# Kernel tuning notes

Measured on AMD Instinct MI355X. Metric: run time of the kernel, lower is better.

The kernel has to match this reference:

```python
import jax, jax.numpy as jnp
import numpy as np

N = 64       # number of sites / qubits
CHI = 32     # bond dimension chi_max
D = 2        # physical dim (== label dim l)
BATCH = 262144
STD = 0.001  # init noise, matches MPS.initialize_params


def setup_inputs() -> dict:
    key = jax.random.key(0)
    kx, k0, kc, kn = jax.random.split(key, 4)
    # X: [N, batch, d] -- each X[i] contracts with site i's physical leg
    X = jax.random.normal(kx, (N, BATCH, D), dtype=jnp.float32)
    # core0: (d, chi), one-hot column 0 plus noise
    core0 = jnp.zeros((D, CHI), jnp.float32).at[:, 0].set(1.0)
    core0 = core0 + STD * jax.random.normal(k0, (D, CHI), dtype=jnp.float32)
    # middle cores: (N-1, chi, d, chi), identity stacked over d plus noise
    eye = jnp.eye(CHI, dtype=jnp.float32)                      # (chi, chi)
    mid = jnp.broadcast_to(eye[:, None, :], (CHI, D, CHI))     # (chi, d, chi)
    cores = jnp.broadcast_to(mid, (N - 1, CHI, D, CHI))
    cores = cores + STD * jax.random.normal(kc, (N - 1, CHI, D, CHI), dtype=jnp.float32)
    # coreN: (chi, d), one-hot row 0 plus noise
    coreN = jnp.zeros((CHI, D), jnp.float32).at[0].set(1.0)
    coreN = coreN + STD * jax.random.normal(kn, (CHI, D), dtype=jnp.float32)
    return {"X": X, "core0": core0, "cores": cores, "coreN": coreN}


def reference(X, core0, cores, coreN):
    # Sequential MPS chain contraction:
    #   v <- X[0] @ core0                       (batch, chi)
    #   v <- einsum('ab,bqc,aq->ac', v, core_i, X[i])   for i = 1..N-1
    #   out = |v @ coreN|                       (batch, l)
    v0 = jnp.einsum('aq,qc->ac', X[0], core0)  # (B, chi)

    def step(v, inp):
        x, core = inp  # x: (B, d), core: (chi, d, chi)
        # contract bond then physical leg, keeping only (B, chi) resident
        v_new = jnp.einsum('ab,bqc,aq->ac', v, core, x)
        return v_new, None

    v, _ = jax.lax.scan(step, v0, (X[1:], cores))
    out = jnp.einsum('ac,cq->aq', v, coreN)    # (B, l)
    return jnp.abs(out)
```

## Files before the change

kernel.cpp:

```cpp
#include <hip/hip_runtime.h>
#include <hip/hip_bf16.h>

#define BATCH 262144
#define NSITES 64
#define NJ 4
#define BLOCK_BATCH 256

typedef __attribute__((ext_vector_type(8))) short short8;
typedef __attribute__((ext_vector_type(4))) float f32x4;

__device__ __forceinline__ int qmap(int k) {
  return (((k >> 2) & 1) << 4) | (((k >> 3) & 3) << 2) | (k & 3);
}

__global__ void pack_E(const float* __restrict__ cores, unsigned short* __restrict__ Ep) {
  int idx = blockIdx.x * 256 + threadIdx.x;
  if (idx >= (NSITES - 1) * 2048) return;
  int t = idx & 7;
  int l = (idx >> 3) & 63;
  int f = (idx >> 9) & 3;
  int p = idx >> 11;
  int g = l >> 4, col = l & 15;
  int m = f >> 1, h = f & 1;
  int k = 8 * g + t, c = h * 16 + col;
  int b = qmap(k);
  float val = cores[((p * 32 + b) * 2 + m) * 32 + c] - ((b == c) ? 1.0f : 0.0f);
  __hip_bfloat16 hv = __float2bfloat16(val);
  Ep[idx] = *(unsigned short*)&hv;
}

#define BODYJ(jj, xx0, xx1)                                                     \
  {                                                                             \
    union { short8 s8; __hip_bfloat162 h2[4]; } vb;                             \
    vb.h2[0] = __float22bfloat162_rn(make_float2(v[jj][0], v[jj][1]));          \
    vb.h2[1] = __float22bfloat162_rn(make_float2(v[jj][2], v[jj][3]));          \
    vb.h2[2] = __float22bfloat162_rn(make_float2(v[jj][4], v[jj][5]));          \
    vb.h2[3] = __float22bfloat162_rn(make_float2(v[jj][6], v[jj][7]));          \
    const f32x4 z = {0.f, 0.f, 0.f, 0.f};                                       \
    __builtin_amdgcn_s_setprio(1);                                              \
    f32x4 r0lo = __builtin_amdgcn_mfma_f32_16x16x32_bf16(A0, vb.s8, z, 0, 0, 0); \
    f32x4 r0hi = __builtin_amdgcn_mfma_f32_16x16x32_bf16(A1, vb.s8, z, 0, 0, 0); \
    f32x4 r1lo = __builtin_amdgcn_mfma_f32_16x16x32_bf16(A2, vb.s8, z, 0, 0, 0); \
    f32x4 r1hi = __builtin_amdgcn_mfma_f32_16x16x32_bf16(A3, vb.s8, z, 0, 0, 0); \
    __builtin_amdgcn_s_setprio(0);                                              \
    const float ss = (xx0) + (xx1);                                             \
    _Pragma("unroll") for (int t = 0; t < 4; ++t) {                             \
      v[jj][t] = ss * v[jj][t] + (xx0)*r0lo[t] + (xx1)*r1lo[t];                 \
      v[jj][4 + t] = ss * v[jj][4 + t] + (xx0)*r0hi[t] + (xx1)*r1hi[t];         \
    }                                                                           \
  }

__global__ __launch_bounds__(256, 4) void mps_chain_kernel(
    const float* __restrict__ X, const float* __restrict__ core0,
    const float* __restrict__ coreN, const unsigned short* __restrict__ Ep,
    float* __restrict__ out) {
  const int tid = threadIdx.x;
  const int lane = tid & 63;
  const int wave = tid >> 6;
  const int col = lane & 15;
  const int g = lane >> 4;
  const int abase = blockIdx.x * BLOCK_BATCH + wave * (16 * NJ);

  float c0[2][8];
#pragma unroll
  for (int m = 0; m < 2; ++m)
#pragma unroll
    for (int t = 0; t < 8; ++t) c0[m][t] = core0[m * 32 + qmap(8 * g + t)];

  float v[NJ][8];
#pragma unroll
  for (int jj = 0; jj < NJ; ++jj) {
    const float2 xj = *(const float2*)(X + 2 * (size_t)(abase + jj * 16 + col));
#pragma unroll
    for (int t = 0; t < 8; ++t) v[jj][t] = xj.x * c0[0][t] + xj.y * c0[1][t];
  }

  const char* ep_base = (const char*)Ep + (size_t)lane * 16;
  const float* xs = X + 2 * ((size_t)BATCH + abase + col);

#pragma unroll 1
  for (int s = 1; s < NSITES; ++s) {
    const short8* ep = (const short8*)ep_base;
    const short8 A0 = ep[0], A1 = ep[64], A2 = ep[128], A3 = ep[192];

    float2 xj[NJ];
#pragma unroll
    for (int jj = 0; jj < NJ; ++jj)
      xj[jj] = *(const float2*)(xs + 2 * (jj * 16));

    BODYJ(0, xj[0].x, xj[0].y);
    BODYJ(1, xj[1].x, xj[1].y);
    BODYJ(2, xj[2].x, xj[2].y);
    BODYJ(3, xj[3].x, xj[3].y);

    ep_base += 4096;
    xs += 2 * (size_t)BATCH;
  }

  float cN[8][2];
#pragma unroll
  for (int t = 0; t < 8; ++t) {
    cN[t][0] = coreN[qmap(8 * g + t) * 2 + 0];
    cN[t][1] = coreN[qmap(8 * g + t) * 2 + 1];
  }
#pragma unroll
  for (int jj = 0; jj < NJ; ++jj) {
    float p0 = 0.f, p1 = 0.f;
#pragma unroll
    for (int t = 0; t < 8; ++t) {
      p0 += v[jj][t] * cN[t][0];
      p1 += v[jj][t] * cN[t][1];
    }
    p0 += __shfl_xor(p0, 16);
    p0 += __shfl_xor(p0, 32);
    p1 += __shfl_xor(p1, 16);
    p1 += __shfl_xor(p1, 32);
    if (g == 0) {
      const int a = abase + jj * 16 + col;
      out[2 * a] = fabsf(p0);
      out[2 * a + 1] = fabsf(p1);
    }
  }
}

extern "C" void kernel_launch(void* const* d_in, const int* in_sizes, int n_in,
                              void* d_out, int out_size, void* d_ws, size_t ws_size,
                              hipStream_t stream) {
  const float* X = (const float*)d_in[0];
  const float* core0 = (const float*)d_in[1];
  const float* cores = (const float*)d_in[2];
  const float* coreN = (const float*)d_in[3];
  float* out = (float*)d_out;
  unsigned short* Ep = (unsigned short*)d_ws;

  hipLaunchKernelGGL(pack_E, dim3(((NSITES - 1) * 2048 + 255) / 256), dim3(256), 0, stream,
                     cores, Ep);
  hipLaunchKernelGGL(mps_chain_kernel, dim3(BATCH / BLOCK_BATCH), dim3(256), 0, stream, X,
                     core0, coreN, Ep, out);
}
```

Measured before the change: 99.75 us.

## Double-buffer per-site cores and X into LDS via async global_load_lds

Each wave now prefetches the next site's packed bf16 core fragments and its X values into a per-wave double-buffered LDS region using global_load_lds. A manual vmcnt wait means each iteration only waits for the previous stage's loads. The goal is to hide the global-load latency that the unroll-1 site loop previously exposed on every step. In exchange it adds about 36KB of LDS per block, which may limit occupancy, and it depends on hand-placed waitcnt ordering.

```diff
diff --git a/kernel.cpp b/kernel.cpp
--- a/kernel.cpp
+++ b/kernel.cpp
@@ -29,6 +29,17 @@
   Ep[idx] = *(unsigned short*)&hv;
 }
 
+__device__ __forceinline__ void gll16(const void* g, void* l) {
+  __builtin_amdgcn_global_load_lds(
+      (const __attribute__((address_space(1))) unsigned*)g,
+      (__attribute__((address_space(3))) unsigned*)l, 16, 0, 0);
+}
+__device__ __forceinline__ void gll4(const void* g, void* l) {
+  __builtin_amdgcn_global_load_lds(
+      (const __attribute__((address_space(1))) unsigned*)g,
+      (__attribute__((address_space(3))) unsigned*)l, 4, 0, 0);
+}
+
 #define BODYJ(jj, xx0, xx1)                                                     \
   {                                                                             \
     union { short8 s8; __hip_bfloat162 h2[4]; } vb;                             \
@@ -54,12 +65,27 @@
     const float* __restrict__ X, const float* __restrict__ core0,
     const float* __restrict__ coreN, const unsigned short* __restrict__ Ep,
     float* __restrict__ out) {
+  __shared__ __align__(16) char Lds[4][2][4608];
   const int tid = threadIdx.x;
   const int lane = tid & 63;
   const int wave = tid >> 6;
   const int col = lane & 15;
   const int g = lane >> 4;
   const int abase = blockIdx.x * BLOCK_BATCH + wave * (16 * NJ);
+  const char* Epc = (const char*)Ep;
+  const char* Xc = (const char*)X;
+
+#define STAGE(t_, b_)                                                           \
+  {                                                                             \
+    const char* es_ = Epc + (size_t)((t_)-1) * 4096 + (size_t)lane * 16;        \
+    gll16(es_, &Lds[wave][b_][0]);                                              \
+    gll16(es_ + 1024, &Lds[wave][b_][1024]);                                    \
+    gll16(es_ + 2048, &Lds[wave][b_][2048]);                                    \
+    gll16(es_ + 3072, &Lds[wave][b_][3072]);                                    \
+    const char* xs_ = Xc + ((size_t)(t_)*BATCH + abase + lane) * 8;             \
+    gll4(xs_, &Lds[wave][b_][4096]);                                            \
+    gll4(xs_ + 4, &Lds[wave][b_][4352]);                                        \
+  }
 
   float c0[2][8];
 #pragma unroll
@@ -75,26 +101,32 @@
     for (int t = 0; t < 8; ++t) v[jj][t] = xj.x * c0[0][t] + xj.y * c0[1][t];
   }
 
-  const char* ep_base = (const char*)Ep + (size_t)lane * 16;
-  const float* xs = X + 2 * ((size_t)BATCH + abase + col);
+  STAGE(1, 1);
 
 #pragma unroll 1
   for (int s = 1; s < NSITES; ++s) {
-    const short8* ep = (const short8*)ep_base;
+    const int rb = s & 1;
+    if (s + 1 < NSITES) {
+      STAGE(s + 1, rb ^ 1);
+      asm volatile("s_waitcnt vmcnt(6)" ::: "memory");
+    } else {
+      asm volatile("s_waitcnt vmcnt(0)" ::: "memory");
+    }
+
+    const short8* ep = (const short8*)&Lds[wave][rb][lane * 16];
     const short8 A0 = ep[0], A1 = ep[64], A2 = ep[128], A3 = ep[192];
+    const float* xp = (const float*)&Lds[wave][rb][4096];
+    float xv0[NJ], xv1[NJ];
+#pragma unroll
+    for (int jj = 0; jj < NJ; ++jj) {
+      xv0[jj] = xp[jj * 16 + col];
+      xv1[jj] = xp[64 + jj * 16 + col];
+    }
 
-    float2 xj[NJ];
-#pragma unroll
-    for (int jj = 0; jj < NJ; ++jj)
-      xj[jj] = *(const float2*)(xs + 2 * (jj * 16));
-
-    BODYJ(0, xj[0].x, xj[0].y);
-    BODYJ(1, xj[1].x, xj[1].y);
-    BODYJ(2, xj[2].x, xj[2].y);
-    BODYJ(3, xj[3].x, xj[3].y);
-
-    ep_base += 4096;
-    xs += 2 * (size_t)BATCH;
+    BODYJ(0, xv0[0], xv1[0]);
+    BODYJ(1, xv0[1], xv1[1]);
+    BODYJ(2, xv0[2], xv1[2]);
+    BODYJ(3, xv0[3], xv1[3]);
   }
 
   float cN[8][2];
@@ -121,6 +153,7 @@
       out[2 * a + 1] = fabsf(p1);
     }
   }
+#undef STAGE
 }
 
 extern "C" void kernel_launch(void* const* d_in, const int* in_sizes, int n_in,
```

Measured after the change: 104.4 us. 1.05x slower.

## Prefetch next site's X and vectorize state update with packed float2 math

Applied to the files above, without the earlier changes.

Loads the X inputs for site s+1 at the top of each iteration, so global-load latency overlaps the current site's MFMA and update work rather than stalling before it. The per-lane state is also restructured into float2 vectors so the scale-and-accumulate update can map to packed FP32 instructions (v_pk_fma/v_pk_mul). This costs extra registers for the prefetched values, which may press on the 4-waves occupancy bound. It also issues one redundant clamped load on the last iteration.

```diff
diff --git a/kernel.cpp b/kernel.cpp
--- a/kernel.cpp
+++ b/kernel.cpp
@@ -8,6 +8,10 @@
 
 typedef __attribute__((ext_vector_type(8))) short short8;
 typedef __attribute__((ext_vector_type(4))) float f32x4;
+typedef __attribute__((ext_vector_type(2))) float f32x2;
+
+#define LOH2(r) (__builtin_shufflevector((r), (r), 0, 1))
+#define HIH2(r) (__builtin_shufflevector((r), (r), 2, 3))
 
 __device__ __forceinline__ int qmap(int k) {
   return (((k >> 2) & 1) << 4) | (((k >> 3) & 3) << 2) | (k & 3);
@@ -32,10 +36,10 @@
 #define BODYJ(jj, xx0, xx1)                                                     \
   {                                                                             \
     union { short8 s8; __hip_bfloat162 h2[4]; } vb;                             \
-    vb.h2[0] = __float22bfloat162_rn(make_float2(v[jj][0], v[jj][1]));          \
-    vb.h2[1] = __float22bfloat162_rn(make_float2(v[jj][2], v[jj][3]));          \
-    vb.h2[2] = __float22bfloat162_rn(make_float2(v[jj][4], v[jj][5]));          \
-    vb.h2[3] = __float22bfloat162_rn(make_float2(v[jj][6], v[jj][7]));          \
+    vb.h2[0] = __float22bfloat162_rn(make_float2(w[jj][0][0], w[jj][0][1]));    \
+    vb.h2[1] = __float22bfloat162_rn(make_float2(w[jj][1][0], w[jj][1][1]));    \
+    vb.h2[2] = __float22bfloat162_rn(make_float2(w[jj][2][0], w[jj][2][1]));    \
+    vb.h2[3] = __float22bfloat162_rn(make_float2(w[jj][3][0], w[jj][3][1]));    \
     const f32x4 z = {0.f, 0.f, 0.f, 0.f};                                       \
     __builtin_amdgcn_s_setprio(1);                                              \
     f32x4 r0lo = __builtin_amdgcn_mfma_f32_16x16x32_bf16(A0, vb.s8, z, 0, 0, 0); \
@@ -44,10 +48,11 @@
     f32x4 r1hi = __builtin_amdgcn_mfma_f32_16x16x32_bf16(A3, vb.s8, z, 0, 0, 0); \
     __builtin_amdgcn_s_setprio(0);                                              \
     const float ss = (xx0) + (xx1);                                             \
-    _Pragma("unroll") for (int t = 0; t < 4; ++t) {                             \
-      v[jj][t] = ss * v[jj][t] + (xx0)*r0lo[t] + (xx1)*r1lo[t];                 \
-      v[jj][4 + t] = ss * v[jj][4 + t] + (xx0)*r0hi[t] + (xx1)*r1hi[t];         \
-    }                                                                           \
+    const f32x2 sv = {ss, ss}, x0v = {(xx0), (xx0)}, x1v = {(xx1), (xx1)};      \
+    w[jj][0] = sv * w[jj][0] + x0v * LOH2(r0lo) + x1v * LOH2(r1lo);             \
+    w[jj][1] = sv * w[jj][1] + x0v * HIH2(r0lo) + x1v * HIH2(r1lo);             \
+    w[jj][2] = sv * w[jj][2] + x0v * LOH2(r0hi) + x1v * LOH2(r1hi);             \
+    w[jj][3] = sv * w[jj][3] + x0v * HIH2(r0hi) + x1v * HIH2(r1hi);             \
   }
 
 __global__ __launch_bounds__(256, 4) void mps_chain_kernel(
@@ -67,34 +72,50 @@
 #pragma unroll
     for (int t = 0; t < 8; ++t) c0[m][t] = core0[m * 32 + qmap(8 * g + t)];
 
-  float v[NJ][8];
+  f32x2 w[NJ][4];
 #pragma unroll
   for (int jj = 0; jj < NJ; ++jj) {
     const float2 xj = *(const float2*)(X + 2 * (size_t)(abase + jj * 16 + col));
 #pragma unroll
-    for (int t = 0; t < 8; ++t) v[jj][t] = xj.x * c0[0][t] + xj.y * c0[1][t];
+    for (int q = 0; q < 4; ++q) {
+      w[jj][q][0] = xj.x * c0[0][2 * q] + xj.y * c0[1][2 * q];
+      w[jj][q][1] = xj.x * c0[0][2 * q + 1] + xj.y * c0[1][2 * q + 1];
+    }
+  }
+
+  const float* xs = X + 2 * (size_t)(abase + col);
+  float xl[NJ], xh[NJ];
+#pragma unroll
+  for (int jj = 0; jj < NJ; ++jj) {
+    const float2 t_ = *(const float2*)(xs + 2 * ((size_t)BATCH + jj * 16));
+    xl[jj] = t_.x;
+    xh[jj] = t_.y;
   }
 
   const char* ep_base = (const char*)Ep + (size_t)lane * 16;
-  const float* xs = X + 2 * ((size_t)BATCH + abase + col);
 
 #pragma unroll 1
   for (int s = 1; s < NSITES; ++s) {
+    const size_t sx = (s + 1 < NSITES) ? (size_t)(s + 1) : (size_t)(NSITES - 1);
+    float2 xn[NJ];
+#pragma unroll
+    for (int jj = 0; jj < NJ; ++jj)
+      xn[jj] = *(const float2*)(xs + 2 * (sx * BATCH + jj * 16));
+
     const short8* ep = (const short8*)ep_base;
     const short8 A0 = ep[0], A1 = ep[64], A2 = ep[128], A3 = ep[192];
 
-    float2 xj[NJ];
+    BODYJ(0, xl[0], xh[0]);
+    BODYJ(1, xl[1], xh[1]);
+    BODYJ(2, xl[2], xh[2]);
+    BODYJ(3, xl[3], xh[3]);
+
 #pragma unroll
-    for (int jj = 0; jj < NJ; ++jj)
-      xj[jj] = *(const float2*)(xs + 2 * (jj * 16));
-
-    BODYJ(0, xj[0].x, xj[0].y);
-    BODYJ(1, xj[1].x, xj[1].y);
-    BODYJ(2, xj[2].x, xj[2].y);
-    BODYJ(3, xj[3].x, xj[3].y);
-
+    for (int jj = 0; jj < NJ; ++jj) {
+      xl[jj] = xn[jj].x;
+      xh[jj] = xn[jj].y;
+    }
     ep_base += 4096;
-    xs += 2 * (size_t)BATCH;
   }
 
   float cN[8][2];
@@ -108,8 +129,8 @@
     float p0 = 0.f, p1 = 0.f;
 #pragma unroll
     for (int t = 0; t < 8; ++t) {
-      p0 += v[jj][t] * cN[t][0];
-      p1 += v[jj][t] * cN[t][1];
+      p0 += w[jj][t >> 1][t & 1] * cN[t][0];
+      p1 += w[jj][t >> 1][t & 1] * cN[t][1];
     }
     p0 += __shfl_xor(p0, 16);
     p0 += __shfl_xor(p0, 32);
```

Result: slower. 101.9 us (+2.1%).

## Double-buffer core and X tiles in LDS via async global-to-LDS loads

Applied to the files above, without the earlier changes.

Replaces the per-site direct global loads of packed cores and X with a double-buffered LDS pipeline. Each epoch stages two sites' worth of core and X data using global_load_lds, then computes on the other buffer. The goal is to overlap memory latency with the MFMA chain and to share core loads across waves. In exchange it adds a block-wide barrier and a vmcnt(0) wait per epoch, plus 24KB of LDS per block, which may reduce occupancy.

```diff
diff --git a/kernel.cpp b/kernel.cpp
--- a/kernel.cpp
+++ b/kernel.cpp
@@ -29,6 +29,12 @@
   Ep[idx] = *(unsigned short*)&hv;
 }
 
+__device__ __forceinline__ void gll16(const void* g, void* l) {
+  __builtin_amdgcn_global_load_lds(
+      (const __attribute__((address_space(1))) unsigned*)g,
+      (__attribute__((address_space(3))) unsigned*)l, 16, 0, 0);
+}
+
 #define BODYJ(jj, xx0, xx1)                                                     \
   {                                                                             \
     union { short8 s8; __hip_bfloat162 h2[4]; } vb;                             \
@@ -50,16 +56,50 @@
     }                                                                           \
   }
 
+#define STEP(buf_, k_)                                                          \
+  {                                                                             \
+    const short8* ep = (const short8*)&Elds[buf_][k_][lane * 16];               \
+    const short8 A0 = ep[0], A1 = ep[64], A2 = ep[128], A3 = ep[192];           \
+    const float* xq = (const float*)&Xlds[buf_][k_][(wave * 64 + col) * 8];     \
+    const float2 x0j = *(const float2*)(xq);                                    \
+    const float2 x1j = *(const float2*)(xq + 32);                               \
+    const float2 x2j = *(const float2*)(xq + 64);                               \
+    const float2 x3j = *(const float2*)(xq + 96);                               \
+    BODYJ(0, x0j.x, x0j.y);                                                     \
+    BODYJ(1, x1j.x, x1j.y);                                                     \
+    BODYJ(2, x2j.x, x2j.y);                                                     \
+    BODYJ(3, x3j.x, x3j.y);                                                     \
+  }
+
 __global__ __launch_bounds__(256, 4) void mps_chain_kernel(
     const float* __restrict__ X, const float* __restrict__ core0,
     const float* __restrict__ coreN, const unsigned short* __restrict__ Ep,
     float* __restrict__ out) {
+  __shared__ __align__(16) char Elds[2][2][4096];
+  __shared__ __align__(16) char Xlds[2][2][2048];
   const int tid = threadIdx.x;
   const int lane = tid & 63;
   const int wave = tid >> 6;
   const int col = lane & 15;
   const int g = lane >> 4;
-  const int abase = blockIdx.x * BLOCK_BATCH + wave * (16 * NJ);
+  const int bb = blockIdx.x * BLOCK_BATCH;
+  const int abase = bb + wave * (16 * NJ);
+  const char* Epc = (const char*)Ep;
+  const char* Xc = (const char*)X;
+  const int xp_ = wave >> 1;
+  const int xkb = wave & 1;
+
+#define STAGE_EPOCH(s0_, b_)                                                    \
+  {                                                                             \
+    int p0_ = (s0_)-1, p1_ = (s0_);                                             \
+    if (p1_ > 62) p1_ = 62;                                                     \
+    gll16(Epc + (size_t)p0_ * 4096 + (size_t)tid * 16, &Elds[b_][0][wave * 1024]); \
+    gll16(Epc + (size_t)p1_ * 4096 + (size_t)tid * 16, &Elds[b_][1][wave * 1024]); \
+    int xs_ = (s0_) + xp_;                                                      \
+    if (xs_ > 63) xs_ = 63;                                                     \
+    gll16(Xc + ((size_t)xs_ * BATCH + bb + xkb * 128) * 8 + (size_t)lane * 16,  \
+          &Xlds[b_][xp_][xkb * 1024]);                                          \
+  }
 
   float c0[2][8];
 #pragma unroll
@@ -75,27 +115,21 @@
     for (int t = 0; t < 8; ++t) v[jj][t] = xj.x * c0[0][t] + xj.y * c0[1][t];
   }
 
-  const char* ep_base = (const char*)Ep + (size_t)lane * 16;
-  const float* xs = X + 2 * ((size_t)BATCH + abase + col);
+  STAGE_EPOCH(1, 0);
+  asm volatile("s_waitcnt vmcnt(0)" ::: "memory");
+  __builtin_amdgcn_s_barrier();
 
 #pragma unroll 1
-  for (int s = 1; s < NSITES; ++s) {
-    const short8* ep = (const short8*)ep_base;
-    const short8 A0 = ep[0], A1 = ep[64], A2 = ep[128], A3 = ep[192];
+  for (int e = 0; e <= 30; ++e) {
+    const int b = e & 1;
+    STAGE_EPOCH(2 * e + 3, b ^ 1);
+    STEP(b, 0);
+    STEP(b, 1);
+    asm volatile("s_waitcnt vmcnt(0)" ::: "memory");
+    __builtin_amdgcn_s_barrier();
+  }
 
-    float2 xj[NJ];
-#pragma unroll
-    for (int jj = 0; jj < NJ; ++jj)
-      xj[jj] = *(const float2*)(xs + 2 * (jj * 16));
-
-    BODYJ(0, xj[0].x, xj[0].y);
-    BODYJ(1, xj[1].x, xj[1].y);
-    BODYJ(2, xj[2].x, xj[2].y);
-    BODYJ(3, xj[3].x, xj[3].y);
-
-    ep_base += 4096;
-    xs += 2 * (size_t)BATCH;
-  }
+  STEP(1, 0);
 
   float cN[8][2];
 #pragma unroll
@@ -121,6 +155,7 @@
       out[2 * a + 1] = fabsf(p1);
     }
   }
+#undef STAGE_EPOCH
 }
 
 extern "C" void kernel_launch(void* const* d_in, const int* in_sizes, int n_in,
```

Result: slower. 139.0 us (+39.3%).
